# Kernel optimization log

Measured on AMD Instinct MI355X. Metric: run time of the kernel, lower is better.

Reference implementation:

```python
import jax, jax.numpy as jnp
import numpy as np

N = 100000      # atoms
E = 200000      # bonds (directed)
N2 = 200000     # 2-set super-nodes
A = 400000      # assignment entries atoms->2-sets
E2 = 400000     # 2-set graph edges
G = 5000        # molecules
D = 256         # emb_dim
FEAT = 40       # num_atom_features
NI2 = 8         # num_i_2
NBOND = 4       # bond types for edge embedding
L = 5           # num_layer
BN_EPS = 1e-5


def setup_inputs() -> dict:
    key = jax.random.key(0)
    ks = jax.random.split(key, 24)
    nrm = lambda k, shape, fan: jax.random.normal(k, shape, jnp.float32) / np.float32(np.sqrt(fan))
    inp = {}
    inp['x'] = jax.random.normal(ks[0], (N, FEAT), jnp.float32)
    inp['edge_index'] = jax.random.randint(ks[1], (2, E), 0, N, jnp.int32)
    inp['edge_attr'] = jax.random.randint(ks[2], (E,), 0, NBOND, jnp.int32)
    inp['iso_type_2'] = jax.random.uniform(ks[3], (N2, NI2), jnp.float32)
    inp['edge_index_2'] = jax.random.randint(ks[4], (2, E2), 0, N2, jnp.int32)
    inp['assignment_index_2'] = jnp.stack([
        jax.random.randint(ks[5], (A,), 0, N, jnp.int32),
        jax.random.randint(ks[6], (A,), 0, N2, jnp.int32)])
    inp['batch'] = jnp.sort(jax.random.randint(ks[7], (N,), 0, G, jnp.int32))
    inp['batch_2'] = jnp.sort(jax.random.randint(ks[8], (N2,), 0, G, jnp.int32))
    # params
    inp['W_emb'] = nrm(ks[9], (FEAT, D), FEAT); inp['b_emb'] = jnp.zeros((D,), jnp.float32)
    inp['edge_tables'] = nrm(ks[10], (L, NBOND, D), D)
    inp['eps'] = jnp.zeros((L,), jnp.float32)
    inp['gin_w1'] = nrm(ks[11], (L, D, 2 * D), D); inp['gin_b1'] = jnp.zeros((L, 2 * D), jnp.float32)
    inp['gin_w2'] = nrm(ks[12], (L, 2 * D, D), 2 * D); inp['gin_b2'] = jnp.zeros((L, D), jnp.float32)
    inp['bn_gamma'] = jnp.ones((L, D), jnp.float32); inp['bn_beta'] = jnp.zeros((L, D), jnp.float32)
    inp['iso1_ws'] = nrm(ks[13], (D + NI2, D), D + NI2)
    inp['iso1_wn'] = nrm(ks[14], (D + NI2, D), D + NI2)
    inp['iso1_b'] = jnp.zeros((D,), jnp.float32)
    inp['iso2_ws'] = nrm(ks[15], (D, D), D)
    inp['iso2_wn'] = nrm(ks[16], (D, D), D)
    inp['iso2_b'] = jnp.zeros((D,), jnp.float32)
    inp['fc0_w'] = nrm(ks[17], (2 * D, D), 2 * D); inp['fc0_b'] = jnp.zeros((D,), jnp.float32)
    inp['fc1_w'] = nrm(ks[18], (D, D // 2), D); inp['fc1_b'] = jnp.zeros((D // 2,), jnp.float32)
    inp['fc2_w'] = nrm(ks[19], (D // 2, D // 4), D // 2); inp['fc2_b'] = jnp.zeros((D // 4,), jnp.float32)
    inp['last_w'] = nrm(ks[20], (D // 4, 1), D // 4); inp['last_b'] = jnp.zeros((1,), jnp.float32)
    return inp


def _segment_mean(v, seg, num):
    s = jax.ops.segment_sum(v, seg, num_segments=num)
    c = jax.ops.segment_sum(jnp.ones((v.shape[0], 1), v.dtype), seg, num_segments=num)
    return s / jnp.maximum(c, 1.0)


def _graph_conv(h, src, dst, ws, wn, b, n):
    # PyG GraphConv: W_self x_i + sum_{j->i} W_nei x_j + b
    nei = jax.ops.segment_sum((h @ wn)[src], dst, num_segments=n)
    return h @ ws + nei + b


def reference(x, edge_index, edge_attr, iso_type_2, edge_index_2, assignment_index_2,
              batch, batch_2, W_emb, b_emb, edge_tables, eps, gin_w1, gin_b1,
              gin_w2, gin_b2, bn_gamma, bn_beta, iso1_ws, iso1_wn, iso1_b,
              iso2_ws, iso2_wn, iso2_b, fc0_w, fc0_b, fc1_w, fc1_b, fc2_w, fc2_b,
              last_w, last_b):
    n = x.shape[0]
    src, dst = edge_index[0], edge_index[1]
    # atom embedding
    h = jax.nn.relu(x @ W_emb + b_emb)
    # GIN stack (JK='last', eval mode: dropout identity, BN with batch stats)
    for l in range(L):
        msg = h[src] + edge_tables[l][edge_attr]          # [E, D]
        agg = jax.ops.segment_sum(msg, dst, num_segments=n)
        z = (1.0 + eps[l]) * h + agg
        z = jax.nn.relu(z @ gin_w1[l] + gin_b1[l]) @ gin_w2[l] + gin_b2[l]
        mu = z.mean(axis=0)
        var = z.var(axis=0)
        z = bn_gamma[l] * (z - mu) * jax.lax.rsqrt(var + BN_EPS) + bn_beta[l]
        h = z if l == L - 1 else jax.nn.relu(z)
    node_rep = h                                           # [N, D]
    # graph pooling (mean)
    x_1 = _segment_mean(node_rep, batch, G)                # [G, D]
    # avg_pool onto 2-set nodes
    xp = _segment_mean(node_rep[assignment_index_2[0]], assignment_index_2[1], N2)
    x2 = jnp.concatenate([xp, iso_type_2], axis=1)         # [N2, D+NI2]
    s2, d2 = edge_index_2[0], edge_index_2[1]
    x2 = jax.nn.relu(_graph_conv(x2, s2, d2, iso1_ws, iso1_wn, iso1_b, N2))
    x2 = jax.nn.relu(_graph_conv(x2, s2, d2, iso2_ws, iso2_wn, iso2_b, N2))
    x_2 = _segment_mean(x2, batch_2, G)                    # [G, D]
    m = jnp.concatenate([x_1, x_2], axis=1)                # [G, 2D]
    m = jax.nn.relu(m @ fc0_w + fc0_b)
    m = jax.nn.relu(m @ fc1_w + fc1_b)
    m = jax.nn.relu(m @ fc2_w + fc2_b)
    m = m @ last_w + last_b
    return m.reshape(-1)                                   # num_tasks == 1
```

## Files before the change

### kernel.cpp

```cpp
#include <hip/hip_runtime.h>
#include <cstddef>

constexpr int NA   = 100000;
constexpr int NE   = 200000;
constexpr int NN2  = 200000;
constexpr int NASS = 400000;
constexpr int NE2  = 400000;
constexpr int NG   = 5000;
constexpr int D    = 256;
constexpr int FEAT = 40;
constexpr int NI2  = 8;
constexpr int NL   = 5;
constexpr int CH   = 25000;

typedef unsigned short u16;
typedef __attribute__((ext_vector_type(8))) short bf16x8;
typedef __attribute__((ext_vector_type(4))) float f32x4;

static __device__ __forceinline__ float b2f(u16 s) {
    union { unsigned int u; float f; } v; v.u = ((unsigned int)s) << 16; return v.f;
}
static __device__ __forceinline__ u16 f2b(float f) {
    union { unsigned int u; float f; } v; v.f = f;
    unsigned int r = v.u + 0x7FFFu + ((v.u >> 16) & 1u);
    return (u16)(r >> 16);
}

constexpr size_t ZB_OFF   = 0;
constexpr size_t TC_OFF   = 51200000;
constexpr size_t XEMB_OFF = 51200000;
constexpr size_t HB_OFF   = 102400000;
constexpr size_t XPB_OFF  = 0;
constexpr size_t HN_OFF   = 102400000;
constexpr size_t MB_OFF   = 204800000;
constexpr size_t F1_OFF   = 215040000;
constexpr size_t F2_OFF   = 220160000;
constexpr size_t F3_OFF   = 222720000;
constexpr size_t WEMT_OFF = 224000000;
constexpr size_t GW1T_OFF = 224065536;
constexpr size_t GW2T_OFF = 226686976;
constexpr size_t IWT_OFF  = 229308416;
constexpr size_t EOFF_OFF = 230400000;
constexpr size_t EIDS_OFF = 230800768;
constexpr size_t AOFF_OFF = 231600832;
constexpr size_t AIDS_OFF = 232400896;
constexpr size_t E2OFF_OFF= 234000960;
constexpr size_t E2IDS_OFF= 234801024;
constexpr size_t CUR_OFF  = 236401088;
constexpr size_t PART_OFF = 237201152;
constexpr size_t GST_OFF  = 237202240;
constexpr size_t G2ST_OFF = 237222272;
constexpr size_t BS_OFF   = 237242304;
constexpr size_t SCL_OFF  = 237244416;
constexpr size_t SHL_OFF  = 237249536;
constexpr size_t WS_BYTES = 237254656;

template<int BIAS, int RELU, int ISO, int ALO, int CSPLIT>
__global__ __launch_bounds__(512) void k_mgemm(
    const u16* __restrict__ A, int lda,
    const u16* __restrict__ Bt,
    const float* __restrict__ bias,
    const float* __restrict__ iso,
    const float* __restrict__ wtail,
    u16* __restrict__ C, int ldc, long clo,
    int M, int N, int K)
{
    __shared__ __align__(16) u16 Ah[128][40];
    __shared__ __align__(16) u16 Al[ALO ? 128 : 1][40];
    __shared__ __align__(16) u16 Bh[256][40];
    __shared__ __align__(16) u16 Bl[256][40];
    const int tid = threadIdx.x;
    const int wave = tid >> 6, lane = tid & 63;
    const int wr = wave >> 2, wc = wave & 3;
    const int bm = blockIdx.y * 128, bn = blockIdx.x * 256;
    const int l15 = lane & 15, lhi = lane >> 4;
    const int ar = tid >> 2, ac = (tid & 3) << 3;
    const u16* Alo = A + (size_t)M * lda;
    const u16* Blo = Bt + (size_t)N * K;
    f32x4 acc[4][4] = {};
    const int ktiles = K >> 5;
    for (int kt = 0; kt < ktiles; ++kt) {
        const int k0 = kt << 5;
        uint4 avh = {0,0,0,0}, avl = {0,0,0,0};
        if (bm + ar < M) {
            avh = *(const uint4*)(A + (size_t)(bm + ar) * lda + k0 + ac);
            if (ALO) avl = *(const uint4*)(Alo + (size_t)(bm + ar) * lda + k0 + ac);
        }
        uint4 b0h = *(const uint4*)(Bt  + (size_t)(bn + ar) * K + k0 + ac);
        uint4 b1h = *(const uint4*)(Bt  + (size_t)(bn + 128 + ar) * K + k0 + ac);
        uint4 b0l = *(const uint4*)(Blo + (size_t)(bn + ar) * K + k0 + ac);
        uint4 b1l = *(const uint4*)(Blo + (size_t)(bn + 128 + ar) * K + k0 + ac);
        __syncthreads();
        *(uint4*)&Ah[ar][ac] = avh;
        if (ALO) *(uint4*)&Al[ar][ac] = avl;
        *(uint4*)&Bh[ar][ac] = b0h;  *(uint4*)&Bh[128 + ar][ac] = b1h;
        *(uint4*)&Bl[ar][ac] = b0l;  *(uint4*)&Bl[128 + ar][ac] = b1l;
        __syncthreads();
        bf16x8 fah[4], fal[4], fbh[4], fbl[4];
        #pragma unroll
        for (int m = 0; m < 4; ++m) {
            fah[m] = *(const bf16x8*)&Ah[wr * 64 + m * 16 + l15][lhi * 8];
            if (ALO) fal[m] = *(const bf16x8*)&Al[wr * 64 + m * 16 + l15][lhi * 8];
        }
        #pragma unroll
        for (int n = 0; n < 4; ++n) {
            fbh[n] = *(const bf16x8*)&Bh[wc * 64 + n * 16 + l15][lhi * 8];
            fbl[n] = *(const bf16x8*)&Bl[wc * 64 + n * 16 + l15][lhi * 8];
        }
        #pragma unroll
        for (int m = 0; m < 4; ++m)
            #pragma unroll
            for (int n = 0; n < 4; ++n) {
                acc[m][n] = __builtin_amdgcn_mfma_f32_16x16x32_bf16(fbh[n], fah[m], acc[m][n], 0, 0, 0);
                acc[m][n] = __builtin_amdgcn_mfma_f32_16x16x32_bf16(fbl[n], fah[m], acc[m][n], 0, 0, 0);
                if (ALO)
                    acc[m][n] = __builtin_amdgcn_mfma_f32_16x16x32_bf16(fbh[n], fal[m], acc[m][n], 0, 0, 0);
            }
    }
    #pragma unroll
    for (int m = 0; m < 4; ++m) {
        int row = bm + wr * 64 + m * 16 + l15;
        if (row >= M) continue;
        #pragma unroll
        for (int n = 0; n < 4; ++n) {
            int cb = bn + wc * 64 + n * 16 + lhi * 4;
            float vv[4];
            #pragma unroll
            for (int r = 0; r < 4; ++r) vv[r] = acc[m][n][r];
            if (BIAS) {
                float4 bv = *(const float4*)(bias + cb);
                vv[0] += bv.x; vv[1] += bv.y; vv[2] += bv.z; vv[3] += bv.w;
            }
            if (ISO) {
                const float* ir = iso + (size_t)row * NI2;
                #pragma unroll
                for (int k = 0; k < NI2; ++k) {
                    float4 wv = *(const float4*)(wtail + k * 256 + cb);
                    float ik = ir[k];
                    vv[0] += ik * wv.x; vv[1] += ik * wv.y;
                    vv[2] += ik * wv.z; vv[3] += ik * wv.w;
                }
            }
            if (RELU) {
                vv[0] = fmaxf(vv[0], 0.f); vv[1] = fmaxf(vv[1], 0.f);
                vv[2] = fmaxf(vv[2], 0.f); vv[3] = fmaxf(vv[3], 0.f);
            }
            ushort4 hv;
            hv.x = f2b(vv[0]); hv.y = f2b(vv[1]); hv.z = f2b(vv[2]); hv.w = f2b(vv[3]);
            size_t cidx = (size_t)row * ldc + cb;
            *(ushort4*)(C + cidx) = hv;
            if (CSPLIT) {
                ushort4 lv;
                lv.x = f2b(vv[0] - b2f(hv.x)); lv.y = f2b(vv[1] - b2f(hv.y));
                lv.z = f2b(vv[2] - b2f(hv.z)); lv.w = f2b(vv[3] - b2f(hv.w));
                *(ushort4*)(C + clo + cidx) = lv;
            }
        }
    }
}

__global__ __launch_bounds__(256) void k_gemm(
    const float* __restrict__ A, int lda,
    const float* __restrict__ B, int ldb,
    const float* __restrict__ bias,
    float* __restrict__ C, int ldc,
    int M, int N, int K, int relu)
{
    __shared__ __align__(16) float As[16][68];
    __shared__ __align__(16) float Bs[16][68];
    const int tid = threadIdx.x;
    const int tx = tid & 15, ty = tid >> 4;
    const int bm = blockIdx.y * 64, bn = blockIdx.x * 64;
    const int arow = tid >> 2, akq = (tid & 3) << 2;
    const int bk = tid >> 4, bnq = (tid & 15) << 2;
    float c[4][4] = {};
    const int ktiles = (K + 15) >> 4;
    for (int kt = 0; kt < ktiles; ++kt) {
        const int k0 = kt << 4;
        float4 av = make_float4(0.f, 0.f, 0.f, 0.f);
        if (bm + arow < M && k0 + akq + 4 <= K)
            av = *reinterpret_cast<const float4*>(A + (size_t)(bm + arow) * lda + (k0 + akq));
        As[akq + 0][arow] = av.x; As[akq + 1][arow] = av.y;
        As[akq + 2][arow] = av.z; As[akq + 3][arow] = av.w;
        float4 bv = make_float4(0.f, 0.f, 0.f, 0.f);
        if (k0 + bk < K && bn + bnq + 4 <= N)
            bv = *reinterpret_cast<const float4*>(B + (size_t)(k0 + bk) * ldb + (bn + bnq));
        *reinterpret_cast<float4*>(&Bs[bk][bnq]) = bv;
        __syncthreads();
        #pragma unroll
        for (int k = 0; k < 16; ++k) {
            float a0 = As[k][ty*4+0], a1 = As[k][ty*4+1], a2 = As[k][ty*4+2], a3 = As[k][ty*4+3];
            float b0 = Bs[k][tx*4+0], b1 = Bs[k][tx*4+1], b2 = Bs[k][tx*4+2], b3 = Bs[k][tx*4+3];
            c[0][0]+=a0*b0;c[0][1]+=a0*b1;c[0][2]+=a0*b2;c[0][3]+=a0*b3;
            c[1][0]+=a1*b0;c[1][1]+=a1*b1;c[1][2]+=a1*b2;c[1][3]+=a1*b3;
            c[2][0]+=a2*b0;c[2][1]+=a2*b1;c[2][2]+=a2*b2;c[2][3]+=a2*b3;
            c[3][0]+=a3*b0;c[3][1]+=a3*b1;c[3][2]+=a3*b2;c[3][3]+=a3*b3;
        }
        __syncthreads();
    }
    #pragma unroll
    for (int i = 0; i < 4; ++i) {
        int row = bm + ty * 4 + i;
        if (row >= M) continue;
        #pragma unroll
        for (int j = 0; j < 4; ++j) {
            int col = bn + tx * 4 + j;
            if (col >= N) continue;
            float v = c[i][j] + bias[col];
            if (relu) v = fmaxf(v, 0.f);
            C[(size_t)row * ldc + col] = v;
        }
    }
}

__global__ void k_zero(float* __restrict__ p, size_t n) {
    size_t i = (size_t)blockIdx.x * blockDim.x + threadIdx.x;
    size_t st = (size_t)gridDim.x * blockDim.x;
    for (; i < n; i += st) p[i] = 0.f;
}
__global__ void k_fill(float* __restrict__ p, int n, float v) {
    int i = blockIdx.x * blockDim.x + threadIdx.x;
    int st = gridDim.x * blockDim.x;
    for (; i < n; i += st) p[i] = v;
}

__global__ void k_count(const int* __restrict__ idx, int n, int* __restrict__ cnt) {
    int i = blockIdx.x * blockDim.x + threadIdx.x;
    int st = gridDim.x * blockDim.x;
    for (; i < n; i += st) atomicAdd(&cnt[idx[i]], 1);
}
__global__ void k_scan_partial(const int* __restrict__ cnt, int n, int* __restrict__ part) {
    __shared__ int sm[256];
    int c = blockIdx.x, t = threadIdx.x;
    int base = c * 4096 + t * 16;
    int s = 0;
    #pragma unroll
    for (int j = 0; j < 16; ++j) { int i = base + j; if (i < n) s += cnt[i]; }
    sm[t] = s; __syncthreads();
    for (int o = 128; o; o >>= 1) { if (t < o) sm[t] += sm[t + o]; __syncthreads(); }
    if (t == 0) part[c] = sm[0];
}
__global__ void k_scan_mid(int* __restrict__ part, int nch, int* __restrict__ off, int n) {
    if (threadIdx.x == 0 && blockIdx.x == 0) {
        int run = 0;
        for (int c = 0; c < nch; ++c) { int v = part[c]; part[c] = run; run += v; }
        off[n] = run;
    }
}
__global__ void k_scan_final(const int* __restrict__ cnt, int n, const int* __restrict__ part,
                             int* __restrict__ off) {
    __shared__ int sm[256];
    int c = blockIdx.x, t = threadIdx.x;
    int base = c * 4096 + t * 16;
    int loc[16]; int s = 0;
    #pragma unroll
    for (int j = 0; j < 16; ++j) { int i = base + j; int v = (i < n) ? cnt[i] : 0; loc[j] = s; s += v; }
    sm[t] = s; __syncthreads();
    for (int o = 1; o < 256; o <<= 1) {
        int v = (t >= o) ? sm[t - o] : 0;
        __syncthreads(); sm[t] += v; __syncthreads();
    }
    int tpre = (t == 0) ? 0 : sm[t - 1];
    int cb = part[c];
    #pragma unroll
    for (int j = 0; j < 16; ++j) { int i = base + j; if (i < n) off[i] = cb + tpre + loc[j]; }
}
__global__ void k_fill_csr(const int* __restrict__ idx, const int* __restrict__ pay, int n,
                           const int* __restrict__ off, int* __restrict__ cur, int* __restrict__ ids) {
    int i = blockIdx.x * blockDim.x + threadIdx.x;
    int st = gridDim.x * blockDim.x;
    for (; i < n; i += st) {
        int d = idx[i];
        int p = off[d] + atomicAdd(&cur[d], 1);
        ids[p] = pay[i];
    }
}
__global__ void k_pack(const int* __restrict__ src, const int* __restrict__ attr,
                       int* __restrict__ pk, int n) {
    int i = blockIdx.x * blockDim.x + threadIdx.x;
    int st = gridDim.x * blockDim.x;
    for (; i < n; i += st) pk[i] = (src[i] << 2) | attr[i];
}
__global__ void k_lbound(const int* __restrict__ arr, int n, int nseg, int* __restrict__ st) {
    int g = blockIdx.x * blockDim.x + threadIdx.x;
    if (g > nseg) return;
    int lo = 0, hi = n;
    while (lo < hi) { int mid = (lo + hi) >> 1; if (arr[mid] < g) lo = mid + 1; else hi = mid; }
    st[g] = lo;
}

__global__ void k_wt(const float* __restrict__ w, u16* __restrict__ wt, int K, int N) {
    int i = blockIdx.x * blockDim.x + threadIdx.x;
    int tot = K * N, st = gridDim.x * blockDim.x;
    for (; i < tot; i += st) {
        int n_ = i / K, k = i - n_ * K;
        float v = w[(size_t)k * N + n_];
        u16 h = f2b(v);
        wt[i] = h;
        wt[(size_t)tot + i] = f2b(v - b2f(h));
    }
}
__global__ void k_wembT(const float* __restrict__ w, u16* __restrict__ wt) {
    int i = blockIdx.x * blockDim.x + threadIdx.x;
    if (i >= 256 * 64) return;
    int n_ = i >> 6, k = i & 63;
    float v = (k < FEAT) ? w[(size_t)k * 256 + n_] : 0.f;
    u16 h = f2b(v);
    wt[i] = h;
    wt[256 * 64 + i] = f2b(v - b2f(h));
}
__global__ void k_xemb(const float* __restrict__ x, u16* __restrict__ xe) {
    size_t i = (size_t)blockIdx.x * blockDim.x + threadIdx.x;
    size_t st = (size_t)gridDim.x * blockDim.x;
    size_t tot = (size_t)NA * 64;
    for (; i < tot; i += st) {
        int r = (int)(i >> 6), c = (int)(i & 63);
        float v = (c < FEAT) ? x[(size_t)r * FEAT + c] : 0.f;
        u16 h = f2b(v);
        xe[i] = h;
        xe[tot + i] = f2b(v - b2f(h));
    }
}

__global__ void k_gin_gather(const u16* __restrict__ hb, const int* __restrict__ off,
                             const int* __restrict__ ids, const float* __restrict__ etab_l,
                             const float* __restrict__ epsv, int l, u16* __restrict__ zb) {
    int wid = (blockIdx.x * blockDim.x + threadIdx.x) >> 6;
    int lane = threadIdx.x & 63;
    int nw = (gridDim.x * blockDim.x) >> 6;
    int c = lane * 4;
    float e1 = 1.f + epsv[l];
    for (int v = wid; v < NA; v += nw) {
        ushort4 h = *(const ushort4*)(hb + (size_t)v * D + c);
        float s0 = e1 * b2f(h.x), s1 = e1 * b2f(h.y), s2 = e1 * b2f(h.z), s3 = e1 * b2f(h.w);
        int p1 = off[v + 1];
        for (int p = off[v]; p < p1; ++p) {
            int pk = ids[p]; int src = pk >> 2; int at = pk & 3;
            ushort4 u = *(const ushort4*)(hb + (size_t)src * D + c);
            float4 t = *(const float4*)(etab_l + at * D + c);
            s0 += b2f(u.x) + t.x; s1 += b2f(u.y) + t.y;
            s2 += b2f(u.z) + t.z; s3 += b2f(u.w) + t.w;
        }
        ushort4 o; o.x = f2b(s0); o.y = f2b(s1); o.z = f2b(s2); o.w = f2b(s3);
        *(ushort4*)(zb + (size_t)v * D + c) = o;
    }
}
__global__ void k_xp_gather(const u16* __restrict__ hb, const int* __restrict__ off,
                            const int* __restrict__ ids, u16* __restrict__ xpb) {
    int wid = (blockIdx.x * blockDim.x + threadIdx.x) >> 6;
    int lane = threadIdx.x & 63;
    int nw = (gridDim.x * blockDim.x) >> 6;
    int c = lane * 4;
    for (int v = wid; v < NN2; v += nw) {
        int p0 = off[v], p1 = off[v + 1];
        float s0 = 0, s1 = 0, s2 = 0, s3 = 0;
        for (int p = p0; p < p1; ++p) {
            ushort4 u = *(const ushort4*)(hb + (size_t)ids[p] * D + c);
            s0 += b2f(u.x); s1 += b2f(u.y); s2 += b2f(u.z); s3 += b2f(u.w);
        }
        float inv = 1.f / fmaxf((float)(p1 - p0), 1.f);
        ushort4 o;
        o.x = f2b(s0 * inv); o.y = f2b(s1 * inv); o.z = f2b(s2 * inv); o.w = f2b(s3 * inv);
        *(ushort4*)(xpb + (size_t)v * D + c) = o;
    }
}
__global__ void k_conv_gather(u16* __restrict__ selfb, const u16* __restrict__ hn,
                              const int* __restrict__ off, const int* __restrict__ ids) {
    int wid = (blockIdx.x * blockDim.x + threadIdx.x) >> 6;
    int lane = threadIdx.x & 63;
    int nw = (gridDim.x * blockDim.x) >> 6;
    int c = lane * 4;
    for (int v = wid; v < NN2; v += nw) {
        ushort4 sv = *(const ushort4*)(selfb + (size_t)v * D + c);
        float s0 = b2f(sv.x), s1 = b2f(sv.y), s2 = b2f(sv.z), s3 = b2f(sv.w);
        int p1 = off[v + 1];
        for (int p = off[v]; p < p1; ++p) {
            ushort4 u = *(const ushort4*)(hn + (size_t)ids[p] * D + c);
            s0 += b2f(u.x); s1 += b2f(u.y); s2 += b2f(u.z); s3 += b2f(u.w);
        }
        ushort4 o;
        o.x = f2b(fmaxf(s0, 0.f)); o.y = f2b(fmaxf(s1, 0.f));
        o.z = f2b(fmaxf(s2, 0.f)); o.w = f2b(fmaxf(s3, 0.f));
        *(ushort4*)(selfb + (size_t)v * D + c) = o;
    }
}

__global__ void k_bn_stats(const u16* __restrict__ zhi, const u16* __restrict__ zlo,
                           float* __restrict__ sum, float* __restrict__ sumsq, int n) {
    int c = threadIdx.x;
    float s = 0.f, q = 0.f;
    for (int r = blockIdx.x; r < n; r += gridDim.x) {
        float v = b2f(zhi[(size_t)r * D + c]) + b2f(zlo[(size_t)r * D + c]);
        s += v; q += v * v;
    }
    atomicAdd(&sum[c], s);
    atomicAdd(&sumsq[c], q);
}
__global__ void k_bn_final(const float* __restrict__ sum, const float* __restrict__ sumsq,
                           const float* __restrict__ gamma, const float* __restrict__ beta,
                           float* __restrict__ scale, float* __restrict__ shift, int n) {
    int c = threadIdx.x;
    float mu = sum[c] / (float)n;
    float var = sumsq[c] / (float)n - mu * mu;
    float sc = gamma[c] * rsqrtf(var + 1e-5f);
    scale[c] = sc;
    shift[c] = beta[c] - mu * sc;
}
__global__ void k_bn_apply(u16* __restrict__ zhi, const u16* __restrict__ zlo,
                           const float* __restrict__ scale, const float* __restrict__ shift,
                           size_t n, int relu) {
    size_t i = (size_t)blockIdx.x * blockDim.x + threadIdx.x;
    size_t st = (size_t)gridDim.x * blockDim.x;
    for (; i < n; i += st) {
        int c = (int)(i & (D - 1));
        float z = b2f(zhi[i]) + b2f(zlo[i]);
        float v = scale[c] * z + shift[c];
        if (relu) v = fmaxf(v, 0.f);
        zhi[i] = f2b(v);
    }
}

__global__ void k_pool1(const u16* __restrict__ hb, const int* __restrict__ gst,
                        float* __restrict__ mb) {
    int g = blockIdx.x, t = threadIdx.x;
    int a = gst[g], b = gst[g + 1];
    float s = 0.f;
    for (int r = a; r < b; ++r) s += b2f(hb[(size_t)r * D + t]);
    mb[(size_t)g * (2 * D) + t] = s / fmaxf((float)(b - a), 1.f);
}
__global__ void k_pool2(const u16* __restrict__ x2b, const int* __restrict__ g2st,
                        float* __restrict__ mb) {
    int g = blockIdx.x, t = threadIdx.x;
    int a = g2st[g], b = g2st[g + 1];
    float s = 0.f;
    for (int r = a; r < b; ++r) s += b2f(x2b[(size_t)r * D + t]);
    mb[(size_t)g * (2 * D) + D + t] = s / fmaxf((float)(b - a), 1.f);
}
__global__ void k_last(const float* __restrict__ f3, const float* __restrict__ w,
                       const float* __restrict__ b, float* __restrict__ out, int gn) {
    int g = blockIdx.x * 4 + (threadIdx.x >> 6);
    int lane = threadIdx.x & 63;
    if (g >= gn) return;
    float v = f3[(size_t)g * 64 + lane] * w[lane];
    #pragma unroll
    for (int off = 32; off; off >>= 1) v += __shfl_down(v, off);
    if (lane == 0) out[g] = v + b[0];
}

static inline dim3 ggrid(int M, int N) { return dim3((N + 63) / 64, (M + 63) / 64); }

extern "C" void kernel_launch(void* const* d_in, const int* in_sizes, int n_in,
                              void* d_out, int out_size, void* d_ws, size_t ws_size,
                              hipStream_t stream) {
    const float* x      = (const float*)d_in[0];
    const int*   eidx   = (const int*)  d_in[1];
    const int*   eattr  = (const int*)  d_in[2];
    const float* iso    = (const float*)d_in[3];
    const int*   eidx2  = (const int*)  d_in[4];
    const int*   assign = (const int*)  d_in[5];
    const int*   batch  = (const int*)  d_in[6];
    const int*   batch2 = (const int*)  d_in[7];
    const float* W_emb  = (const float*)d_in[8];
    const float* b_emb  = (const float*)d_in[9];
    const float* etab   = (const float*)d_in[10];
    const float* epsv   = (const float*)d_in[11];
    const float* gw1    = (const float*)d_in[12];
    const float* gb1    = (const float*)d_in[13];
    const float* gw2    = (const float*)d_in[14];
    const float* gb2    = (const float*)d_in[15];
    const float* bng    = (const float*)d_in[16];
    const float* bnb    = (const float*)d_in[17];
    const float* i1ws   = (const float*)d_in[18];
    const float* i1wn   = (const float*)d_in[19];
    const float* i1b    = (const float*)d_in[20];
    const float* i2ws   = (const float*)d_in[21];
    const float* i2wn   = (const float*)d_in[22];
    const float* i2b    = (const float*)d_in[23];
    const float* fc0w   = (const float*)d_in[24];
    const float* fc0b   = (const float*)d_in[25];
    const float* fc1w   = (const float*)d_in[26];
    const float* fc1b   = (const float*)d_in[27];
    const float* fc2w   = (const float*)d_in[28];
    const float* fc2b   = (const float*)d_in[29];
    const float* lw     = (const float*)d_in[30];
    const float* lb     = (const float*)d_in[31];

    float* out = (float*)d_out;
    char*  ws  = (char*)d_ws;
    if (ws_size < WS_BYTES) {
        k_fill<<<32, 256, 0, stream>>>(out, out_size, 10000.0f + (float)(ws_size >> 20));
        return;
    }

    u16*   ZB   = (u16*)(ws + ZB_OFF);
    u16*   TC   = (u16*)(ws + TC_OFF);
    u16*   XEMB = (u16*)(ws + XEMB_OFF);
    u16*   HB   = (u16*)(ws + HB_OFF);
    u16*   XPB  = (u16*)(ws + XPB_OFF);
    u16*   HN   = (u16*)(ws + HN_OFF);
    float* Mb   = (float*)(ws + MB_OFF);
    float* F1   = (float*)(ws + F1_OFF);
    float* F2   = (float*)(ws + F2_OFF);
    float* F3   = (float*)(ws + F3_OFF);
    u16*   wembT= (u16*)(ws + WEMT_OFF);
    u16*   gw1T = (u16*)(ws + GW1T_OFF);
    u16*   gw2T = (u16*)(ws + GW2T_OFF);
    u16*   iwT  = (u16*)(ws + IWT_OFF);
    u16*   i1wnT= iwT;
    u16*   i1wsT= iwT + 2 * 65536;
    u16*   i2wnT= iwT + 4 * 65536;
    u16*   i2wsT= iwT + 6 * 65536;
    int*   eoff = (int*)(ws + EOFF_OFF);
    int*   eids = (int*)(ws + EIDS_OFF);
    int*   aoff = (int*)(ws + AOFF_OFF);
    int*   aids = (int*)(ws + AIDS_OFF);
    int*   e2off= (int*)(ws + E2OFF_OFF);
    int*   e2ids= (int*)(ws + E2IDS_OFF);
    int*   cur  = (int*)(ws + CUR_OFF);
    int*   part = (int*)(ws + PART_OFF);
    int*   gst  = (int*)(ws + GST_OFF);
    int*   g2st = (int*)(ws + G2ST_OFF);
    float* BS   = (float*)(ws + BS_OFF);
    float* SCL  = (float*)(ws + SCL_OFF);
    float* SHL  = (float*)(ws + SHL_OFF);
    int*   packs= (int*)F1;

    const int* e_src = eidx;   const int* e_dst = eidx + NE;
    const int* a0    = assign; const int* a1    = assign + NASS;
    const int* s2    = eidx2;  const int* d2    = eidx2 + NE2;

    u16* HBlo = HB + (size_t)NA * D;

    dim3 sg(2048);
    dim3 ew(8192);
    const int nchA = (NA + 4095) / 4096;
    const int nch2 = (NN2 + 4095) / 4096;

    k_lbound<<<dim3((NG + 256) / 256), 256, 0, stream>>>(batch, NA, NG, gst);
    k_lbound<<<dim3((NG + 256) / 256), 256, 0, stream>>>(batch2, NN2, NG, g2st);

    k_zero<<<dim3(256), 256, 0, stream>>>((float*)cur, NA);
    k_count<<<dim3(1024), 256, 0, stream>>>(e_dst, NE, cur);
    k_scan_partial<<<dim3(nchA), 256, 0, stream>>>(cur, NA, part);
    k_scan_mid<<<dim3(1), 64, 0, stream>>>(part, nchA, eoff, NA);
    k_scan_final<<<dim3(nchA), 256, 0, stream>>>(cur, NA, part, eoff);
    k_zero<<<dim3(256), 256, 0, stream>>>((float*)cur, NA);
    k_pack<<<dim3(1024), 256, 0, stream>>>(e_src, eattr, packs, NE);
    k_fill_csr<<<dim3(1024), 256, 0, stream>>>(e_dst, packs, NE, eoff, cur, eids);

    k_zero<<<dim3(256), 256, 0, stream>>>((float*)cur, NN2);
    k_count<<<dim3(1024), 256, 0, stream>>>(a1, NASS, cur);
    k_scan_partial<<<dim3(nch2), 256, 0, stream>>>(cur, NN2, part);
    k_scan_mid<<<dim3(1), 64, 0, stream>>>(part, nch2, aoff, NN2);
    k_scan_final<<<dim3(nch2), 256, 0, stream>>>(cur, NN2, part, aoff);
    k_zero<<<dim3(256), 256, 0, stream>>>((float*)cur, NN2);
    k_fill_csr<<<dim3(1024), 256, 0, stream>>>(a1, a0, NASS, aoff, cur, aids);

    k_zero<<<dim3(256), 256, 0, stream>>>((float*)cur, NN2);
    k_count<<<dim3(1024), 256, 0, stream>>>(d2, NE2, cur);
    k_scan_partial<<<dim3(nch2), 256, 0, stream>>>(cur, NN2, part);
    k_scan_mid<<<dim3(1), 64, 0, stream>>>(part, nch2, e2off, NN2);
    k_scan_final<<<dim3(nch2), 256, 0, stream>>>(cur, NN2, part, e2off);
    k_zero<<<dim3(256), 256, 0, stream>>>((float*)cur, NN2);
    k_fill_csr<<<dim3(1024), 256, 0, stream>>>(d2, s2, NE2, e2off, cur, e2ids);

    k_wembT<<<dim3(64), 256, 0, stream>>>(W_emb, wembT);
    for (int l = 0; l < NL; ++l) {
        k_wt<<<dim3(512), 256, 0, stream>>>(gw1 + (size_t)l * D * 2 * D, gw1T + (size_t)l * 2 * 2 * D * D, D, 2 * D);
        k_wt<<<dim3(512), 256, 0, stream>>>(gw2 + (size_t)l * 2 * D * D, gw2T + (size_t)l * 2 * 2 * D * D, 2 * D, D);
    }
    k_wt<<<dim3(256), 256, 0, stream>>>(i1wn, i1wnT, D, D);
    k_wt<<<dim3(256), 256, 0, stream>>>(i1ws, i1wsT, D, D);
    k_wt<<<dim3(256), 256, 0, stream>>>(i2wn, i2wnT, D, D);
    k_wt<<<dim3(256), 256, 0, stream>>>(i2ws, i2wsT, D, D);

    k_xemb<<<ew, 256, 0, stream>>>(x, XEMB);
    k_mgemm<1,1,0,1,0><<<dim3(1, (NA + 127) / 128), 512, 0, stream>>>(
        XEMB, 64, wembT, b_emb, nullptr, nullptr, HB, D, 0, NA, D, 64);

    for (int l = 0; l < NL; ++l) {
        k_gin_gather<<<sg, 256, 0, stream>>>(HB, eoff, eids, etab + (size_t)l * 4 * D, epsv, l, ZB);
        for (int c = 0; c < NA / CH; ++c) {
            k_mgemm<1,1,0,0,1><<<dim3(2, (CH + 127) / 128), 512, 0, stream>>>(
                ZB + (size_t)c * CH * D, D, gw1T + (size_t)l * 2 * 2 * D * D,
                gb1 + (size_t)l * 2 * D, nullptr, nullptr,
                TC, 2 * D, (long)CH * 2 * D, CH, 2 * D, D);
            k_mgemm<1,0,0,1,1><<<dim3(1, (CH + 127) / 128), 512, 0, stream>>>(
                TC, 2 * D, gw2T + (size_t)l * 2 * 2 * D * D,
                gb2 + (size_t)l * D, nullptr, nullptr,
                HB + (size_t)c * CH * D, D, (long)NA * D, CH, D, 2 * D);
        }
        k_zero<<<dim3(1), 512, 0, stream>>>(BS, 512);
        k_bn_stats<<<dim3(512), 256, 0, stream>>>(HB, HBlo, BS, BS + D, NA);
        k_bn_final<<<dim3(1), 256, 0, stream>>>(BS, BS + D, bng + (size_t)l * D, bnb + (size_t)l * D,
                                                SCL + l * D, SHL + l * D, NA);
        k_bn_apply<<<ew, 256, 0, stream>>>(HB, HBlo, SCL + l * D, SHL + l * D,
                                           (size_t)NA * D, l < NL - 1 ? 1 : 0);
    }

    k_pool1<<<dim3(NG), 256, 0, stream>>>(HB, gst, Mb);

    k_xp_gather<<<sg, 256, 0, stream>>>(HB, aoff, aids, XPB);

    k_mgemm<0,0,1,0,0><<<dim3(1, (NN2 + 127) / 128), 512, 0, stream>>>(
        XPB, D, i1wnT, nullptr, iso, i1wn + (size_t)D * D, HN, D, 0, NN2, D, D);
    k_mgemm<1,0,1,0,0><<<dim3(1, (NN2 + 127) / 128), 512, 0, stream>>>(
        XPB, D, i1wsT, i1b, iso, i1ws + (size_t)D * D, XPB, D, 0, NN2, D, D);
    k_conv_gather<<<sg, 256, 0, stream>>>(XPB, HN, e2off, e2ids);

    k_mgemm<0,0,0,0,0><<<dim3(1, (NN2 + 127) / 128), 512, 0, stream>>>(
        XPB, D, i2wnT, nullptr, nullptr, nullptr, HN, D, 0, NN2, D, D);
    k_mgemm<1,0,0,0,0><<<dim3(1, (NN2 + 127) / 128), 512, 0, stream>>>(
        XPB, D, i2wsT, i2b, nullptr, nullptr, XPB, D, 0, NN2, D, D);
    k_conv_gather<<<sg, 256, 0, stream>>>(XPB, HN, e2off, e2ids);

    k_pool2<<<dim3(NG), 256, 0, stream>>>(XPB, g2st, Mb);

    k_gemm<<<ggrid(NG, D), 256, 0, stream>>>(Mb, 2 * D, fc0w, D, fc0b, F1, D, NG, D, 2 * D, 1);
    k_gemm<<<ggrid(NG, D / 2), 256, 0, stream>>>(F1, D, fc1w, D / 2, fc1b, F2, D / 2, NG, D / 2, D, 1);
    k_gemm<<<ggrid(NG, D / 4), 256, 0, stream>>>(F2, D / 2, fc2w, D / 4, fc2b, F3, D / 4, NG, D / 4, D / 2, 1);
    k_last<<<dim3((NG + 3) / 4), 256, 0, stream>>>(F3, lw, lb, out, NG);
}
```

Measured before the change: 3.270 ms.

## Fuse dual graph-conv GEMMs and use 64-row tiles for GIN MLP GEMMs

Adds a k_mdual kernel that computes the neighbour-weight and self-weight products of each graph-conv layer in one launch. A single staged A tile is shared by two 4-wave groups, each with its own B matrix, which removes one full read of the 200k-row activation matrix and one launch per layer. The GIN MLP GEMMs now run with a 64-row, 256-thread tile variant of k_mgemm, giving about twice as many blocks for the 25k-row chunks so more compute units are busy. The trade-off is heavier per-block LDS use in the dual kernel (about 86 KB) and more redundant B loads per row in the smaller tiles.

```diff
diff --git a/kernel.cpp b/kernel.cpp
--- a/kernel.cpp
+++ b/kernel.cpp
@@ -55,8 +55,8 @@
 constexpr size_t SHL_OFF  = 237249536;
 constexpr size_t WS_BYTES = 237254656;
 
-template<int BIAS, int RELU, int ISO, int ALO, int CSPLIT>
-__global__ __launch_bounds__(512) void k_mgemm(
+template<int BIAS, int RELU, int ISO, int ALO, int CSPLIT, int BM128>
+__global__ __launch_bounds__(BM128 ? 512 : 256) void k_mgemm(
     const u16* __restrict__ A, int lda,
     const u16* __restrict__ Bt,
     const float* __restrict__ bias,
@@ -65,14 +65,17 @@
     u16* __restrict__ C, int ldc, long clo,
     int M, int N, int K)
 {
-    __shared__ __align__(16) u16 Ah[128][40];
-    __shared__ __align__(16) u16 Al[ALO ? 128 : 1][40];
+    constexpr int BM = BM128 ? 128 : 64;
+    constexpr int NB = 256 / BM;
+    __shared__ __align__(16) u16 Ah[BM][40];
+    __shared__ __align__(16) u16 Al[ALO ? BM : 1][40];
     __shared__ __align__(16) u16 Bh[256][40];
     __shared__ __align__(16) u16 Bl[256][40];
     const int tid = threadIdx.x;
     const int wave = tid >> 6, lane = tid & 63;
-    const int wr = wave >> 2, wc = wave & 3;
-    const int bm = blockIdx.y * 128, bn = blockIdx.x * 256;
+    const int wr = BM128 ? (wave >> 2) : 0;
+    const int wc = BM128 ? (wave & 3) : wave;
+    const int bm = blockIdx.y * BM, bn = blockIdx.x * 256;
     const int l15 = lane & 15, lhi = lane >> 4;
     const int ar = tid >> 2, ac = (tid & 3) << 3;
     const u16* Alo = A + (size_t)M * lda;
@@ -86,21 +89,27 @@
             avh = *(const uint4*)(A + (size_t)(bm + ar) * lda + k0 + ac);
             if (ALO) avl = *(const uint4*)(Alo + (size_t)(bm + ar) * lda + k0 + ac);
         }
-        uint4 b0h = *(const uint4*)(Bt  + (size_t)(bn + ar) * K + k0 + ac);
-        uint4 b1h = *(const uint4*)(Bt  + (size_t)(bn + 128 + ar) * K + k0 + ac);
-        uint4 b0l = *(const uint4*)(Blo + (size_t)(bn + ar) * K + k0 + ac);
-        uint4 b1l = *(const uint4*)(Blo + (size_t)(bn + 128 + ar) * K + k0 + ac);
+        uint4 bhr[NB], blr[NB];
+        #pragma unroll
+        for (int i = 0; i < NB; ++i) {
+            bhr[i] = *(const uint4*)(Bt  + (size_t)(bn + i * BM + ar) * K + k0 + ac);
+            blr[i] = *(const uint4*)(Blo + (size_t)(bn + i * BM + ar) * K + k0 + ac);
+        }
         __syncthreads();
         *(uint4*)&Ah[ar][ac] = avh;
         if (ALO) *(uint4*)&Al[ar][ac] = avl;
-        *(uint4*)&Bh[ar][ac] = b0h;  *(uint4*)&Bh[128 + ar][ac] = b1h;
-        *(uint4*)&Bl[ar][ac] = b0l;  *(uint4*)&Bl[128 + ar][ac] = b1l;
+        #pragma unroll
+        for (int i = 0; i < NB; ++i) {
+            *(uint4*)&Bh[i * BM + ar][ac] = bhr[i];
+            *(uint4*)&Bl[i * BM + ar][ac] = blr[i];
+        }
         __syncthreads();
         bf16x8 fah[4], fal[4], fbh[4], fbl[4];
         #pragma unroll
         for (int m = 0; m < 4; ++m) {
-            fah[m] = *(const bf16x8*)&Ah[wr * 64 + m * 16 + l15][lhi * 8];
-            if (ALO) fal[m] = *(const bf16x8*)&Al[wr * 64 + m * 16 + l15][lhi * 8];
+            int arow = (BM128 ? wr * 64 : 0) + m * 16 + l15;
+            fah[m] = *(const bf16x8*)&Ah[arow][lhi * 8];
+            if (ALO) fal[m] = *(const bf16x8*)&Al[arow][lhi * 8];
         }
         #pragma unroll
         for (int n = 0; n < 4; ++n) {
@@ -119,7 +128,7 @@
     }
     #pragma unroll
     for (int m = 0; m < 4; ++m) {
-        int row = bm + wr * 64 + m * 16 + l15;
+        int row = bm + (BM128 ? wr * 64 : 0) + m * 16 + l15;
         if (row >= M) continue;
         #pragma unroll
         for (int n = 0; n < 4; ++n) {
@@ -155,6 +164,110 @@
                 lv.z = f2b(vv[2] - b2f(hv.z)); lv.w = f2b(vv[3] - b2f(hv.w));
                 *(ushort4*)(C + clo + cidx) = lv;
             }
+        }
+    }
+}
+
+template<int ISO>
+__global__ __launch_bounds__(512) void k_mdual(
+    const u16* __restrict__ A,
+    const u16* __restrict__ B0t,
+    const u16* __restrict__ B1t,
+    const float* __restrict__ bias1,
+    const float* __restrict__ iso,
+    const float* __restrict__ wtail0,
+    const float* __restrict__ wtail1,
+    u16* __restrict__ C0,
+    u16* __restrict__ C1,
+    int M)
+{
+    __shared__ __align__(16) u16 Ah[64][40];
+    __shared__ __align__(16) u16 B0h[256][40];
+    __shared__ __align__(16) u16 B0l[256][40];
+    __shared__ __align__(16) u16 B1h[256][40];
+    __shared__ __align__(16) u16 B1l[256][40];
+    const int tid = threadIdx.x;
+    const int wave = tid >> 6, lane = tid & 63;
+    const int osel = wave >> 2, wc = wave & 3;
+    const int bm = blockIdx.x * 64;
+    const int l15 = lane & 15, lhi = lane >> 4;
+    const int sar = tid >> 3, sac = (tid & 7) << 2;
+    const int sbr = tid >> 2, sbc = (tid & 3) << 3;
+    const u16* B0lo = B0t + 256 * 256;
+    const u16* B1lo = B1t + 256 * 256;
+    f32x4 acc[4][4] = {};
+    for (int kt = 0; kt < 8; ++kt) {
+        const int k0 = kt << 5;
+        ushort4 av = {0,0,0,0};
+        if (bm + sar < M) av = *(const ushort4*)(A + (size_t)(bm + sar) * 256 + k0 + sac);
+        uint4 v0h[2], v0l[2], v1h[2], v1l[2];
+        #pragma unroll
+        for (int i = 0; i < 2; ++i) {
+            size_t brow = (size_t)(i * 128 + sbr) * 256 + k0 + sbc;
+            v0h[i] = *(const uint4*)(B0t  + brow);
+            v0l[i] = *(const uint4*)(B0lo + brow);
+            v1h[i] = *(const uint4*)(B1t  + brow);
+            v1l[i] = *(const uint4*)(B1lo + brow);
+        }
+        __syncthreads();
+        *(ushort4*)&Ah[sar][sac] = av;
+        #pragma unroll
+        for (int i = 0; i < 2; ++i) {
+            *(uint4*)&B0h[i * 128 + sbr][sbc] = v0h[i];
+            *(uint4*)&B0l[i * 128 + sbr][sbc] = v0l[i];
+            *(uint4*)&B1h[i * 128 + sbr][sbc] = v1h[i];
+            *(uint4*)&B1l[i * 128 + sbr][sbc] = v1l[i];
+        }
+        __syncthreads();
+        const u16 (*Bhs)[40] = osel ? B1h : B0h;
+        const u16 (*Bls)[40] = osel ? B1l : B0l;
+        bf16x8 fah[4], fbh[4], fbl[4];
+        #pragma unroll
+        for (int m = 0; m < 4; ++m)
+            fah[m] = *(const bf16x8*)&Ah[m * 16 + l15][lhi * 8];
+        #pragma unroll
+        for (int n = 0; n < 4; ++n) {
+            fbh[n] = *(const bf16x8*)&Bhs[wc * 64 + n * 16 + l15][lhi * 8];
+            fbl[n] = *(const bf16x8*)&Bls[wc * 64 + n * 16 + l15][lhi * 8];
+        }
+        #pragma unroll
+        for (int m = 0; m < 4; ++m)
+            #pragma unroll
+            for (int n = 0; n < 4; ++n) {
+                acc[m][n] = __builtin_amdgcn_mfma_f32_16x16x32_bf16(fbh[n], fah[m], acc[m][n], 0, 0, 0);
+                acc[m][n] = __builtin_amdgcn_mfma_f32_16x16x32_bf16(fbl[n], fah[m], acc[m][n], 0, 0, 0);
+            }
+    }
+    u16* C = osel ? C1 : C0;
+    const float* bias = osel ? bias1 : nullptr;
+    const float* wt = osel ? wtail1 : wtail0;
+    #pragma unroll
+    for (int m = 0; m < 4; ++m) {
+        int row = bm + m * 16 + l15;
+        if (row >= M) continue;
+        #pragma unroll
+        for (int n = 0; n < 4; ++n) {
+            int cb = wc * 64 + n * 16 + lhi * 4;
+            float vv[4];
+            #pragma unroll
+            for (int r = 0; r < 4; ++r) vv[r] = acc[m][n][r];
+            if (bias) {
+                float4 bv = *(const float4*)(bias + cb);
+                vv[0] += bv.x; vv[1] += bv.y; vv[2] += bv.z; vv[3] += bv.w;
+            }
+            if (ISO) {
+                const float* ir = iso + (size_t)row * NI2;
+                #pragma unroll
+                for (int k = 0; k < NI2; ++k) {
+                    float4 wv = *(const float4*)(wt + k * 256 + cb);
+                    float ik = ir[k];
+                    vv[0] += ik * wv.x; vv[1] += ik * wv.y;
+                    vv[2] += ik * wv.z; vv[3] += ik * wv.w;
+                }
+            }
+            ushort4 hv;
+            hv.x = f2b(vv[0]); hv.y = f2b(vv[1]); hv.z = f2b(vv[2]); hv.w = f2b(vv[3]);
+            *(ushort4*)(C + (size_t)row * 256 + cb) = hv;
         }
     }
 }
@@ -575,17 +688,18 @@
     k_wt<<<dim3(256), 256, 0, stream>>>(i2ws, i2wsT, D, D);
 
     k_xemb<<<ew, 256, 0, stream>>>(x, XEMB);
-    k_mgemm<1,1,0,1,0><<<dim3(1, (NA + 127) / 128), 512, 0, stream>>>(
+    k_mgemm<1,1,0,1,0,1><<<dim3(1, (NA + 127) / 128), 512, 0, stream>>>(
         XEMB, 64, wembT, b_emb, nullptr, nullptr, HB, D, 0, NA, D, 64);
 
+    const int gy = (CH + 63) / 64;
     for (int l = 0; l < NL; ++l) {
         k_gin_gather<<<sg, 256, 0, stream>>>(HB, eoff, eids, etab + (size_t)l * 4 * D, epsv, l, ZB);
         for (int c = 0; c < NA / CH; ++c) {
-            k_mgemm<1,1,0,0,1><<<dim3(2, (CH + 127) / 128), 512, 0, stream>>>(
+            k_mgemm<1,1,0,0,1,0><<<dim3(2, gy), 256, 0, stream>>>(
                 ZB + (size_t)c * CH * D, D, gw1T + (size_t)l * 2 * 2 * D * D,
                 gb1 + (size_t)l * 2 * D, nullptr, nullptr,
                 TC, 2 * D, (long)CH * 2 * D, CH, 2 * D, D);
-            k_mgemm<1,0,0,1,1><<<dim3(1, (CH + 127) / 128), 512, 0, stream>>>(
+            k_mgemm<1,0,0,1,1,0><<<dim3(1, gy), 256, 0, stream>>>(
                 TC, 2 * D, gw2T + (size_t)l * 2 * 2 * D * D,
                 gb2 + (size_t)l * D, nullptr, nullptr,
                 HB + (size_t)c * CH * D, D, (long)NA * D, CH, D, 2 * D);
@@ -602,16 +716,12 @@
 
     k_xp_gather<<<sg, 256, 0, stream>>>(HB, aoff, aids, XPB);
 
-    k_mgemm<0,0,1,0,0><<<dim3(1, (NN2 + 127) / 128), 512, 0, stream>>>(
-        XPB, D, i1wnT, nullptr, iso, i1wn + (size_t)D * D, HN, D, 0, NN2, D, D);
-    k_mgemm<1,0,1,0,0><<<dim3(1, (NN2 + 127) / 128), 512, 0, stream>>>(
-        XPB, D, i1wsT, i1b, iso, i1ws + (size_t)D * D, XPB, D, 0, NN2, D, D);
+    k_mdual<1><<<dim3(NN2 / 64), 512, 0, stream>>>(
+        XPB, i1wnT, i1wsT, i1b, iso, i1wn + (size_t)D * D, i1ws + (size_t)D * D, HN, XPB, NN2);
     k_conv_gather<<<sg, 256, 0, stream>>>(XPB, HN, e2off, e2ids);
 
-    k_mgemm<0,0,0,0,0><<<dim3(1, (NN2 + 127) / 128), 512, 0, stream>>>(
-        XPB, D, i2wnT, nullptr, nullptr, nullptr, HN, D, 0, NN2, D, D);
-    k_mgemm<1,0,0,0,0><<<dim3(1, (NN2 + 127) / 128), 512, 0, stream>>>(
-        XPB, D, i2wsT, i2b, nullptr, nullptr, XPB, D, 0, NN2, D, D);
+    k_mdual<0><<<dim3(NN2 / 64), 512, 0, stream>>>(
+        XPB, i2wnT, i2wsT, i2b, nullptr, nullptr, nullptr, HN, XPB, NN2);
     k_conv_gather<<<sg, 256, 0, stream>>>(XPB, HN, e2off, e2ids);
 
     k_pool2<<<dim3(NG), 256, 0, stream>>>(XPB, g2st, Mb);
```

New measurement: 5.742 ms. 75.6% more time.
